# Kernel tuning notes

Measured on AMD Instinct MI355X. Metric: run time of the kernel, lower is better.

Reference implementation:

```python
import jax, jax.numpy as jnp
import numpy as np

N_NODES = 100000
N_EDGES = 1600000
N_RELS = 4
F_IN, H_DIM, OUT_DIM = 128, 64, 64
N_LAYERS = 3  # num_hidden_layers=2 h2h layers + 1 h2o layer (all 64->64 here)


def setup_inputs() -> dict:
    key = jax.random.key(0)
    ks = jax.random.split(key, 10)
    h = jax.random.normal(ks[0], (N_NODES, F_IN), dtype=jnp.float32)
    src = jax.random.randint(ks[1], (N_EDGES,), 0, N_NODES, dtype=jnp.int32)
    dst = jax.random.randint(ks[2], (N_EDGES,), 0, N_NODES, dtype=jnp.int32)
    etypes = jax.random.randint(ks[3], (N_EDGES,), 0, N_RELS, dtype=jnp.int32)
    # parameters, scaled ~1/sqrt(fan_in) for numerical sanity through ReLU stack
    W_fc = jax.random.normal(ks[4], (F_IN, H_DIM), dtype=jnp.float32) / np.sqrt(F_IN)
    W_rels = jax.random.normal(ks[5], (N_LAYERS, N_RELS, H_DIM, H_DIM), dtype=jnp.float32) / np.sqrt(H_DIM)
    W_loops = jax.random.normal(ks[6], (N_LAYERS, H_DIM, H_DIM), dtype=jnp.float32) / np.sqrt(H_DIM)
    biases = jnp.zeros((N_LAYERS, H_DIM), dtype=jnp.float32)
    W_dense = jax.random.normal(ks[7], (OUT_DIM, 1), dtype=jnp.float32) / np.sqrt(OUT_DIM)
    b_dense = jnp.zeros((1,), dtype=jnp.float32)
    return {"h": h, "src": src, "dst": dst, "etypes": etypes,
            "W_fc": W_fc, "W_rels": W_rels, "W_loops": W_loops,
            "biases": biases, "W_dense": W_dense, "b_dense": b_dense}


def reference(h, src, dst, etypes, W_fc, W_rels, W_loops, biases, W_dense, b_dense):
    n = h.shape[0]
    # GATLayer.forward returns g.ndata['z'] (fc projection); the attention
    # aggregate written to 'h' by reduce_func is never read in the original.
    x = h @ W_fc  # (N, H)
    # RelGraphConv stack: msg = W_{r(e)} h_src, sum over in-edges, + self-loop + bias, ReLU
    for l in range(N_LAYERS):
        # transform every node under every relation, then gather per edge
        xw = jnp.einsum('nd,rde->rne', x, W_rels[l])        # (R, N, H)
        msg = xw[etypes, src]                                # (E, H)
        agg = jax.ops.segment_sum(msg, dst, num_segments=n)  # (N, H)
        x = jax.nn.relu(agg + x @ W_loops[l] + biases[l])
    # SumPooling over the single graph; h viewed as (N, 1, OUT_DIM)
    pooled = jnp.sum(x.reshape(n, -1, OUT_DIM), axis=0)[None]  # (1, 1, OUT_DIM)
    out = pooled @ W_dense + b_dense                            # (1, 1, 1)
    return out
```

## Files before the change

kernel.cpp:

```cpp
#include <hip/hip_runtime.h>


typedef __attribute__((ext_vector_type(8))) short short8;
typedef __attribute__((ext_vector_type(4))) float f32x4;

__device__ inline unsigned short f32_to_bf16_rne(float x) {
  unsigned u = __builtin_bit_cast(unsigned, x);
  unsigned r = (u + 0x7FFFu + ((u >> 16) & 1u)) >> 16;
  return (unsigned short)r;
}
__device__ inline float bf16_bits_to_f32(unsigned short b) {
  unsigned u = ((unsigned)b) << 16;
  return __builtin_bit_cast(float, u);
}


__global__ void k_degree(const int* __restrict__ dst, int* __restrict__ deg, int E) {
  int i = blockIdx.x * blockDim.x + threadIdx.x;
  if (i < E) atomicAdd(&deg[dst[i]], 1);
}

__global__ __launch_bounds__(1024) void k_scan1(const int* __restrict__ deg,
                                                int* __restrict__ scan,
                                                int* __restrict__ part, int N) {
  __shared__ int s[1024];
  int tid = threadIdx.x;
  int idx = blockIdx.x * 1024 + tid;
  int v = (idx < N) ? deg[idx] : 0;
  s[tid] = v;
  __syncthreads();
  for (int off = 1; off < 1024; off <<= 1) {
    int t = (tid >= off) ? s[tid - off] : 0;
    __syncthreads();
    s[tid] += t;
    __syncthreads();
  }
  if (idx < N) scan[idx] = s[tid];
  if (tid == 1023) part[blockIdx.x] = s[1023];
}

__global__ __launch_bounds__(1024) void k_scan2(const int* __restrict__ part,
                                                int* __restrict__ partx, int nblk) {
  __shared__ int s[1024];
  int tid = threadIdx.x;
  int v = (tid < nblk) ? part[tid] : 0;
  s[tid] = v;
  __syncthreads();
  for (int off = 1; off < 1024; off <<= 1) {
    int t = (tid >= off) ? s[tid - off] : 0;
    __syncthreads();
    s[tid] += t;
    __syncthreads();
  }
  if (tid < nblk) partx[tid] = s[tid] - v;
}

__global__ void k_scan3(const int* __restrict__ scan, const int* __restrict__ deg,
                        const int* __restrict__ partx, int* __restrict__ rowptr,
                        int* __restrict__ cursor, int N, int E) {
  int i = blockIdx.x * blockDim.x + threadIdx.x;
  if (i < N) {
    int v = scan[i] - deg[i] + partx[i >> 10];
    rowptr[i] = v;
    cursor[i] = v;
  }
  if (i == 0) rowptr[N] = E;
}

__global__ void k_scatter(const int* __restrict__ src, const int* __restrict__ dst,
                          const int* __restrict__ et, int* __restrict__ cursor,
                          unsigned* __restrict__ edata, int E) {
  int i = blockIdx.x * blockDim.x + threadIdx.x;
  if (i < E) {
    int d = dst[i];
    int pos = atomicAdd(&cursor[d], 1);
    edata[pos] = (unsigned)src[i] | ((unsigned)et[i] << 17);
  }
}


__global__ __launch_bounds__(256) void k_agg(const int* __restrict__ rowptr,
                                             const unsigned* __restrict__ edata,
                                             const float* __restrict__ x,
                                             float* __restrict__ pre, int N) {
  int wid = (blockIdx.x * blockDim.x + threadIdx.x) >> 6;
  int lane = threadIdx.x & 63;
  if (wid >= N) return;
  int beg = rowptr[wid];
  int end = rowptr[wid + 1];
  float a0 = 0.f, a1 = 0.f, a2 = 0.f, a3 = 0.f;
  int e = beg;
  for (; e + 4 <= end; e += 4) {
    unsigned p0 = __builtin_amdgcn_readfirstlane(edata[e]);
    unsigned p1 = __builtin_amdgcn_readfirstlane(edata[e + 1]);
    unsigned p2 = __builtin_amdgcn_readfirstlane(edata[e + 2]);
    unsigned p3 = __builtin_amdgcn_readfirstlane(edata[e + 3]);
    float v0 = x[(size_t)(p0 & 0x1FFFF) * 64 + lane];
    float v1 = x[(size_t)(p1 & 0x1FFFF) * 64 + lane];
    float v2 = x[(size_t)(p2 & 0x1FFFF) * 64 + lane];
    float v3 = x[(size_t)(p3 & 0x1FFFF) * 64 + lane];
    { int t = p0 >> 17; if (t == 0) a0 += v0; else if (t == 1) a1 += v0; else if (t == 2) a2 += v0; else a3 += v0; }
    { int t = p1 >> 17; if (t == 0) a0 += v1; else if (t == 1) a1 += v1; else if (t == 2) a2 += v1; else a3 += v1; }
    { int t = p2 >> 17; if (t == 0) a0 += v2; else if (t == 1) a1 += v2; else if (t == 2) a2 += v2; else a3 += v2; }
    { int t = p3 >> 17; if (t == 0) a0 += v3; else if (t == 1) a1 += v3; else if (t == 2) a2 += v3; else a3 += v3; }
  }
  for (; e < end; ++e) {
    unsigned p = __builtin_amdgcn_readfirstlane(edata[e]);
    float v = x[(size_t)(p & 0x1FFFF) * 64 + lane];
    int t = p >> 17;
    if (t == 0) a0 += v; else if (t == 1) a1 += v; else if (t == 2) a2 += v; else a3 += v;
  }
  float* o = pre + (size_t)wid * 256 + lane;
  o[0] = a0; o[64] = a1; o[128] = a2; o[192] = a3;
}


__global__ void k_bconv(const float* __restrict__ B0, int K0,
                        const float* __restrict__ B1, int K1,
                        unsigned short* __restrict__ Bh,
                        unsigned short* __restrict__ Bm,
                        unsigned short* __restrict__ Bl) {
  int K = K0 + K1;
  int idx = blockIdx.x * 256 + threadIdx.x;
  if (idx >= K * 64) return;
  int k = idx >> 6, col = idx & 63;
  float v;
  if (k < K0)      v = B0[(size_t)k * 64 + col];
  else if (k < K)  v = B1[(size_t)(k - K0) * 64 + col];
  else             v = 0.f;
  int kstep = k >> 5, kk = k & 31;
  int ct = col >> 4;
  int lane = (col & 15) + (((kk >> 3)) << 4);
  int j = kk & 7;
  size_t o = (((size_t)(kstep * 4 + ct)) * 64 + lane) * 8 + j;
  unsigned short hb = f32_to_bf16_rne(v);
  float r1 = v - bf16_bits_to_f32(hb);
  unsigned short mb = f32_to_bf16_rne(r1);
  unsigned short lb = f32_to_bf16_rne(r1 - bf16_bits_to_f32(mb));
  Bh[o] = hb; Bm[o] = mb; Bl[o] = lb;
}


__global__ __launch_bounds__(256) void k_mgemm(
    const float* __restrict__ A0, int K0,
    const float* __restrict__ A1, int K1,
    const unsigned short* __restrict__ Bh,
    const unsigned short* __restrict__ Bm,
    const unsigned short* __restrict__ Bl,
    const float* __restrict__ bias, int relu,
    float* __restrict__ C, int M,
    const float* __restrict__ Wd, float* __restrict__ accum, int pool) {
  __shared__ short8 Ah[8 * 64], Am[8 * 64], Al[8 * 64];
  __shared__ float red[256];

  const int tid = threadIdx.x;
  const int wave = tid >> 6;
  const int lane = tid & 63;
  const int row0 = blockIdx.x * 128;
  const int K = K0 + K1;

  f32x4 acc[2][4];
#pragma unroll
  for (int i = 0; i < 2; ++i)
#pragma unroll
    for (int j = 0; j < 4; ++j) acc[i][j] = (f32x4){0.f, 0.f, 0.f, 0.f};

  const int srow = tid >> 1;
  const int kk0 = (tid & 1) * 16;
  const int rt_s = srow >> 4;
  const int laneA = (srow & 15) + ((kk0 >> 3) << 4);

  for (int kb = 0; kb < K; kb += 32) {
    {
      const float* Ap;
      int lda;
      if (kb < K0) { Ap = A0 + kb; lda = K0; }
      else         { Ap = A1 + (kb - K0); lda = K1; }
      const int grow = row0 + srow;
      float v[16];
      if (grow < M) {
        const float* s = Ap + (size_t)grow * lda + kk0;
#pragma unroll
        for (int q = 0; q < 4; ++q)
          *reinterpret_cast<float4*>(&v[q * 4]) =
              *reinterpret_cast<const float4*>(s + q * 4);
      } else {
#pragma unroll
        for (int q = 0; q < 16; ++q) v[q] = 0.f;
      }
      short h[16], m[16], l[16];
#pragma unroll
      for (int q = 0; q < 16; ++q) {
        unsigned short hb = f32_to_bf16_rne(v[q]);
        float r1 = v[q] - bf16_bits_to_f32(hb);
        unsigned short mb = f32_to_bf16_rne(r1);
        unsigned short lb = f32_to_bf16_rne(r1 - bf16_bits_to_f32(mb));
        h[q] = (short)hb; m[q] = (short)mb; l[q] = (short)lb;
      }
      short8 H0 = {h[0], h[1], h[2], h[3], h[4], h[5], h[6], h[7]};
      short8 H1 = {h[8], h[9], h[10], h[11], h[12], h[13], h[14], h[15]};
      short8 M0 = {m[0], m[1], m[2], m[3], m[4], m[5], m[6], m[7]};
      short8 M1 = {m[8], m[9], m[10], m[11], m[12], m[13], m[14], m[15]};
      short8 L0 = {l[0], l[1], l[2], l[3], l[4], l[5], l[6], l[7]};
      short8 L1 = {l[8], l[9], l[10], l[11], l[12], l[13], l[14], l[15]};
      Ah[rt_s * 64 + laneA] = H0;
      Ah[rt_s * 64 + laneA + 16] = H1;
      Am[rt_s * 64 + laneA] = M0;
      Am[rt_s * 64 + laneA + 16] = M1;
      Al[rt_s * 64 + laneA] = L0;
      Al[rt_s * 64 + laneA + 16] = L1;
    }
    __syncthreads();

    const int rt0 = wave * 2, rt1 = rt0 + 1;
    short8 ah0 = Ah[rt0 * 64 + lane], ah1 = Ah[rt1 * 64 + lane];
    short8 am0 = Am[rt0 * 64 + lane], am1 = Am[rt1 * 64 + lane];
    short8 al0 = Al[rt0 * 64 + lane], al1 = Al[rt1 * 64 + lane];
    const int kstep = kb >> 5;
#pragma unroll
    for (int ct = 0; ct < 4; ++ct) {
      size_t bo = (((size_t)(kstep * 4 + ct)) * 64 + lane) * 8;
      short8 bh = *reinterpret_cast<const short8*>(&Bh[bo]);
      short8 bm = *reinterpret_cast<const short8*>(&Bm[bo]);
      short8 bl = *reinterpret_cast<const short8*>(&Bl[bo]);
      acc[0][ct] = __builtin_amdgcn_mfma_f32_16x16x32_bf16(ah0, bh, acc[0][ct], 0, 0, 0);
      acc[0][ct] = __builtin_amdgcn_mfma_f32_16x16x32_bf16(ah0, bm, acc[0][ct], 0, 0, 0);
      acc[0][ct] = __builtin_amdgcn_mfma_f32_16x16x32_bf16(am0, bh, acc[0][ct], 0, 0, 0);
      acc[0][ct] = __builtin_amdgcn_mfma_f32_16x16x32_bf16(ah0, bl, acc[0][ct], 0, 0, 0);
      acc[0][ct] = __builtin_amdgcn_mfma_f32_16x16x32_bf16(al0, bh, acc[0][ct], 0, 0, 0);
      acc[0][ct] = __builtin_amdgcn_mfma_f32_16x16x32_bf16(am0, bm, acc[0][ct], 0, 0, 0);
      acc[1][ct] = __builtin_amdgcn_mfma_f32_16x16x32_bf16(ah1, bh, acc[1][ct], 0, 0, 0);
      acc[1][ct] = __builtin_amdgcn_mfma_f32_16x16x32_bf16(ah1, bm, acc[1][ct], 0, 0, 0);
      acc[1][ct] = __builtin_amdgcn_mfma_f32_16x16x32_bf16(am1, bh, acc[1][ct], 0, 0, 0);
      acc[1][ct] = __builtin_amdgcn_mfma_f32_16x16x32_bf16(ah1, bl, acc[1][ct], 0, 0, 0);
      acc[1][ct] = __builtin_amdgcn_mfma_f32_16x16x32_bf16(al1, bh, acc[1][ct], 0, 0, 0);
      acc[1][ct] = __builtin_amdgcn_mfma_f32_16x16x32_bf16(am1, bm, acc[1][ct], 0, 0, 0);
    }
    __syncthreads();
  }

  float local = 0.f;
#pragma unroll
  for (int rt = 0; rt < 2; ++rt) {
#pragma unroll
    for (int ct = 0; ct < 4; ++ct) {
      const int col = ct * 16 + (lane & 15);
      const float bc = bias ? bias[col] : 0.f;
#pragma unroll
      for (int reg = 0; reg < 4; ++reg) {
        const int grow = row0 + wave * 32 + rt * 16 + (lane >> 4) * 4 + reg;
        if (grow < M) {
          float y = acc[rt][ct][reg] + bc;
          if (relu) y = fmaxf(y, 0.f);
          if (pool) local += y * Wd[col];
          else C[(size_t)grow * 64 + col] = y;
        }
      }
    }
  }
  if (pool) {
    red[tid] = local;
    __syncthreads();
    for (int off = 128; off > 0; off >>= 1) {
      if (tid < off) red[tid] += red[tid + off];
      __syncthreads();
    }
    if (tid == 0) atomicAdd(accum, red[0]);
  }
}

__global__ void k_final(const float* __restrict__ accum, const float* __restrict__ b,
                        float* __restrict__ out) {
  out[0] = accum[0] + b[0];
}


extern "C" void kernel_launch(void* const* d_in, const int* in_sizes, int n_in,
                              void* d_out, int out_size, void* d_ws, size_t ws_size,
                              hipStream_t stream) {
  const float* h       = (const float*)d_in[0];
  const int*   src     = (const int*)d_in[1];
  const int*   dst     = (const int*)d_in[2];
  const int*   et      = (const int*)d_in[3];
  const float* W_fc    = (const float*)d_in[4];
  const float* W_rels  = (const float*)d_in[5];
  const float* W_loops = (const float*)d_in[6];
  const float* biases  = (const float*)d_in[7];
  const float* W_dense = (const float*)d_in[8];
  const float* b_dense = (const float*)d_in[9];
  float* out = (float*)d_out;

  const int N = in_sizes[0] / 128;
  const int E = in_sizes[1];

  size_t cur = 0;
  auto carve = [&](size_t bytes) -> char* {
    cur = (cur + 255) & ~(size_t)255;
    char* p = (char*)d_ws + cur;
    cur += bytes;
    return p;
  };
  int* deg        = (int*)carve((size_t)N * 4);
  int* scan       = (int*)carve((size_t)N * 4);
  int* part       = (int*)carve(1024 * 4);
  int* partx      = (int*)carve(1024 * 4);
  int* rowptr     = (int*)carve((size_t)(N + 1) * 4);
  int* cursor     = (int*)carve((size_t)N * 4);
  unsigned* edata = (unsigned*)carve((size_t)E * 4);
  float* xA       = (float*)carve((size_t)N * 64 * 4);
  float* xB       = (float*)carve((size_t)N * 64 * 4);
  float* pre      = (float*)carve((size_t)N * 256 * 4);
  float* accum    = (float*)carve(256);
  unsigned short* Bfc[3];
  for (int p = 0; p < 3; ++p) Bfc[p] = (unsigned short*)carve((size_t)128 * 64 * 2);
  unsigned short* Blay[3][3];
  for (int l = 0; l < 3; ++l)
    for (int p = 0; p < 3; ++p) Blay[l][p] = (unsigned short*)carve((size_t)320 * 64 * 2);

  hipMemsetAsync(deg, 0, (size_t)N * 4, stream);
  hipMemsetAsync(accum, 0, 4, stream);

  k_bconv<<<(128 * 64 + 255) / 256, 256, 0, stream>>>(W_fc, 128, nullptr, 0,
                                                      Bfc[0], Bfc[1], Bfc[2]);
  for (int l = 0; l < 3; ++l)
    k_bconv<<<(320 * 64 + 255) / 256, 256, 0, stream>>>(
        W_rels + (size_t)l * 4 * 64 * 64, 256, W_loops + (size_t)l * 64 * 64, 64,
        Blay[l][0], Blay[l][1], Blay[l][2]);

  const int eb = (E + 255) / 256;
  k_degree<<<eb, 256, 0, stream>>>(dst, deg, E);
  const int nblk = (N + 1023) / 1024;
  k_scan1<<<nblk, 1024, 0, stream>>>(deg, scan, part, N);
  k_scan2<<<1, 1024, 0, stream>>>(part, partx, nblk);
  k_scan3<<<(N + 255) / 256, 256, 0, stream>>>(scan, deg, partx, rowptr, cursor, N, E);
  k_scatter<<<eb, 256, 0, stream>>>(src, dst, et, cursor, edata, E);

  const int gb = (N + 127) / 128;
  k_mgemm<<<gb, 256, 0, stream>>>(h, 128, nullptr, 0,
                                  Bfc[0], Bfc[1], Bfc[2],
                                  nullptr, 0, xA, N, nullptr, nullptr, 0);

  float* xin = xA;
  float* xout = xB;
  for (int l = 0; l < 3; ++l) {
    k_agg<<<(N + 3) / 4, 256, 0, stream>>>(rowptr, edata, xin, pre, N);
    const int last = (l == 2);
    k_mgemm<<<gb, 256, 0, stream>>>(pre, 256, xin, 64,
                                    Blay[l][0], Blay[l][1], Blay[l][2],
                                    biases + (size_t)l * 64, 1,
                                    last ? nullptr : xout, N,
                                    last ? W_dense : nullptr, accum, last);
    float* t = xin; xin = xout; xout = t;
  }

  k_final<<<1, 1, 0, stream>>>(accum, b_dense, out);
}
```

Baseline: 667.6 us.

## Fuse edge aggregation with relation GEMM into one per-layer kernel

```diff
diff --git a/kernel.cpp b/kernel.cpp
--- a/kernel.cpp
+++ b/kernel.cpp
@@ -76,42 +76,6 @@
     int pos = atomicAdd(&cursor[d], 1);
     edata[pos] = (unsigned)src[i] | ((unsigned)et[i] << 17);
   }
-}
-
-
-__global__ __launch_bounds__(256) void k_agg(const int* __restrict__ rowptr,
-                                             const unsigned* __restrict__ edata,
-                                             const float* __restrict__ x,
-                                             float* __restrict__ pre, int N) {
-  int wid = (blockIdx.x * blockDim.x + threadIdx.x) >> 6;
-  int lane = threadIdx.x & 63;
-  if (wid >= N) return;
-  int beg = rowptr[wid];
-  int end = rowptr[wid + 1];
-  float a0 = 0.f, a1 = 0.f, a2 = 0.f, a3 = 0.f;
-  int e = beg;
-  for (; e + 4 <= end; e += 4) {
-    unsigned p0 = __builtin_amdgcn_readfirstlane(edata[e]);
-    unsigned p1 = __builtin_amdgcn_readfirstlane(edata[e + 1]);
-    unsigned p2 = __builtin_amdgcn_readfirstlane(edata[e + 2]);
-    unsigned p3 = __builtin_amdgcn_readfirstlane(edata[e + 3]);
-    float v0 = x[(size_t)(p0 & 0x1FFFF) * 64 + lane];
-    float v1 = x[(size_t)(p1 & 0x1FFFF) * 64 + lane];
-    float v2 = x[(size_t)(p2 & 0x1FFFF) * 64 + lane];
-    float v3 = x[(size_t)(p3 & 0x1FFFF) * 64 + lane];
-    { int t = p0 >> 17; if (t == 0) a0 += v0; else if (t == 1) a1 += v0; else if (t == 2) a2 += v0; else a3 += v0; }
-    { int t = p1 >> 17; if (t == 0) a0 += v1; else if (t == 1) a1 += v1; else if (t == 2) a2 += v1; else a3 += v1; }
-    { int t = p2 >> 17; if (t == 0) a0 += v2; else if (t == 1) a1 += v2; else if (t == 2) a2 += v2; else a3 += v2; }
-    { int t = p3 >> 17; if (t == 0) a0 += v3; else if (t == 1) a1 += v3; else if (t == 2) a2 += v3; else a3 += v3; }
-  }
-  for (; e < end; ++e) {
-    unsigned p = __builtin_amdgcn_readfirstlane(edata[e]);
-    float v = x[(size_t)(p & 0x1FFFF) * 64 + lane];
-    int t = p >> 17;
-    if (t == 0) a0 += v; else if (t == 1) a1 += v; else if (t == 2) a2 += v; else a3 += v;
-  }
-  float* o = pre + (size_t)wid * 256 + lane;
-  o[0] = a0; o[64] = a1; o[128] = a2; o[192] = a3;
 }
 
 
@@ -141,23 +105,132 @@
 }
 
 
-__global__ __launch_bounds__(256) void k_mgemm(
-    const float* __restrict__ A0, int K0,
-    const float* __restrict__ A1, int K1,
+__global__ __launch_bounds__(256) void k_fused(
+    const int* __restrict__ rowptr, const unsigned* __restrict__ edata,
+    const float* __restrict__ x,
     const unsigned short* __restrict__ Bh,
     const unsigned short* __restrict__ Bm,
     const unsigned short* __restrict__ Bl,
-    const float* __restrict__ bias, int relu,
-    float* __restrict__ C, int M,
+    const float* __restrict__ bias,
+    float* __restrict__ xout, int N,
     const float* __restrict__ Wd, float* __restrict__ accum, int pool) {
+  __shared__ float A[16][324];
+  __shared__ float red[256];
+
+  const int tid = threadIdx.x;
+  const int wave = tid >> 6;
+  const int lane = tid & 63;
+  const int node0 = blockIdx.x * 16;
+
+  for (int i = 0; i < 4; ++i) {
+    const int r = wave * 4 + i;
+    const int n = node0 + r;
+    float a0 = 0.f, a1 = 0.f, a2 = 0.f, a3 = 0.f, xs = 0.f;
+    if (n < N) {
+      int beg = rowptr[n];
+      int end = rowptr[n + 1];
+      int e = beg;
+      for (; e + 4 <= end; e += 4) {
+        unsigned p0 = __builtin_amdgcn_readfirstlane(edata[e]);
+        unsigned p1 = __builtin_amdgcn_readfirstlane(edata[e + 1]);
+        unsigned p2 = __builtin_amdgcn_readfirstlane(edata[e + 2]);
+        unsigned p3 = __builtin_amdgcn_readfirstlane(edata[e + 3]);
+        float v0 = x[(size_t)(p0 & 0x1FFFF) * 64 + lane];
+        float v1 = x[(size_t)(p1 & 0x1FFFF) * 64 + lane];
+        float v2 = x[(size_t)(p2 & 0x1FFFF) * 64 + lane];
+        float v3 = x[(size_t)(p3 & 0x1FFFF) * 64 + lane];
+        { int t = p0 >> 17; if (t == 0) a0 += v0; else if (t == 1) a1 += v0; else if (t == 2) a2 += v0; else a3 += v0; }
+        { int t = p1 >> 17; if (t == 0) a0 += v1; else if (t == 1) a1 += v1; else if (t == 2) a2 += v1; else a3 += v1; }
+        { int t = p2 >> 17; if (t == 0) a0 += v2; else if (t == 1) a1 += v2; else if (t == 2) a2 += v2; else a3 += v2; }
+        { int t = p3 >> 17; if (t == 0) a0 += v3; else if (t == 1) a1 += v3; else if (t == 2) a2 += v3; else a3 += v3; }
+      }
+      for (; e < end; ++e) {
+        unsigned p = __builtin_amdgcn_readfirstlane(edata[e]);
+        float v = x[(size_t)(p & 0x1FFFF) * 64 + lane];
+        int t = p >> 17;
+        if (t == 0) a0 += v; else if (t == 1) a1 += v; else if (t == 2) a2 += v; else a3 += v;
+      }
+      xs = x[(size_t)n * 64 + lane];
+    }
+    A[r][0 * 64 + lane] = a0;
+    A[r][1 * 64 + lane] = a1;
+    A[r][2 * 64 + lane] = a2;
+    A[r][3 * 64 + lane] = a3;
+    A[r][256 + lane] = xs;
+  }
+  __syncthreads();
+
+  f32x4 acc = (f32x4){0.f, 0.f, 0.f, 0.f};
+  const int arow = lane & 15;
+  const int koff = (lane >> 4) * 8;
+#pragma unroll
+  for (int ks = 0; ks < 10; ++ks) {
+    float av[8];
+    *reinterpret_cast<float4*>(&av[0]) =
+        *reinterpret_cast<const float4*>(&A[arow][ks * 32 + koff]);
+    *reinterpret_cast<float4*>(&av[4]) =
+        *reinterpret_cast<const float4*>(&A[arow][ks * 32 + koff + 4]);
+    short h[8], m[8], l[8];
+#pragma unroll
+    for (int q = 0; q < 8; ++q) {
+      unsigned short hb = f32_to_bf16_rne(av[q]);
+      float r1 = av[q] - bf16_bits_to_f32(hb);
+      unsigned short mb = f32_to_bf16_rne(r1);
+      unsigned short lb = f32_to_bf16_rne(r1 - bf16_bits_to_f32(mb));
+      h[q] = (short)hb; m[q] = (short)mb; l[q] = (short)lb;
+    }
+    short8 ah = {h[0], h[1], h[2], h[3], h[4], h[5], h[6], h[7]};
+    short8 am = {m[0], m[1], m[2], m[3], m[4], m[5], m[6], m[7]};
+    short8 al = {l[0], l[1], l[2], l[3], l[4], l[5], l[6], l[7]};
+    size_t bo = (((size_t)(ks * 4 + wave)) * 64 + lane) * 8;
+    short8 bh = *reinterpret_cast<const short8*>(&Bh[bo]);
+    short8 bm = *reinterpret_cast<const short8*>(&Bm[bo]);
+    short8 bl = *reinterpret_cast<const short8*>(&Bl[bo]);
+    acc = __builtin_amdgcn_mfma_f32_16x16x32_bf16(ah, bh, acc, 0, 0, 0);
+    acc = __builtin_amdgcn_mfma_f32_16x16x32_bf16(ah, bm, acc, 0, 0, 0);
+    acc = __builtin_amdgcn_mfma_f32_16x16x32_bf16(am, bh, acc, 0, 0, 0);
+    acc = __builtin_amdgcn_mfma_f32_16x16x32_bf16(ah, bl, acc, 0, 0, 0);
+    acc = __builtin_amdgcn_mfma_f32_16x16x32_bf16(al, bh, acc, 0, 0, 0);
+    acc = __builtin_amdgcn_mfma_f32_16x16x32_bf16(am, bm, acc, 0, 0, 0);
+  }
+
+  const int col = wave * 16 + (lane & 15);
+  const float bc = bias ? bias[col] : 0.f;
+  float local = 0.f;
+#pragma unroll
+  for (int reg = 0; reg < 4; ++reg) {
+    const int grow = node0 + (lane >> 4) * 4 + reg;
+    if (grow < N) {
+      float y = fmaxf(acc[reg] + bc, 0.f);
+      if (pool) local += y * Wd[col];
+      else xout[(size_t)grow * 64 + col] = y;
+    }
+  }
+  if (pool) {
+    red[tid] = local;
+    __syncthreads();
+    for (int off = 128; off > 0; off >>= 1) {
+      if (tid < off) red[tid] += red[tid + off];
+      __syncthreads();
+    }
+    if (tid == 0) atomicAdd(accum, red[0]);
+  }
+}
+
+
+__global__ __launch_bounds__(256) void k_mgemm(
+    const float* __restrict__ A0, int K0,
+    const unsigned short* __restrict__ Bh,
+    const unsigned short* __restrict__ Bm,
+    const unsigned short* __restrict__ Bl,
+    float* __restrict__ C, int M) {
   __shared__ short8 Ah[8 * 64], Am[8 * 64], Al[8 * 64];
-  __shared__ float red[256];
 
   const int tid = threadIdx.x;
   const int wave = tid >> 6;
   const int lane = tid & 63;
   const int row0 = blockIdx.x * 128;
-  const int K = K0 + K1;
+  const int K = K0;
 
   f32x4 acc[2][4];
 #pragma unroll
@@ -172,14 +245,10 @@
 
   for (int kb = 0; kb < K; kb += 32) {
     {
-      const float* Ap;
-      int lda;
-      if (kb < K0) { Ap = A0 + kb; lda = K0; }
-      else         { Ap = A1 + (kb - K0); lda = K1; }
       const int grow = row0 + srow;
       float v[16];
       if (grow < M) {
-        const float* s = Ap + (size_t)grow * lda + kk0;
+        const float* s = A0 + (size_t)grow * K + kb + kk0;
 #pragma unroll
         for (int q = 0; q < 4; ++q)
           *reinterpret_cast<float4*>(&v[q * 4]) =
@@ -239,33 +308,17 @@
     __syncthreads();
   }
 
-  float local = 0.f;
 #pragma unroll
   for (int rt = 0; rt < 2; ++rt) {
 #pragma unroll
     for (int ct = 0; ct < 4; ++ct) {
       const int col = ct * 16 + (lane & 15);
-      const float bc = bias ? bias[col] : 0.f;
 #pragma unroll
       for (int reg = 0; reg < 4; ++reg) {
         const int grow = row0 + wave * 32 + rt * 16 + (lane >> 4) * 4 + reg;
-        if (grow < M) {
-          float y = acc[rt][ct][reg] + bc;
-          if (relu) y = fmaxf(y, 0.f);
-          if (pool) local += y * Wd[col];
-          else C[(size_t)grow * 64 + col] = y;
-        }
+        if (grow < M) C[(size_t)grow * 64 + col] = acc[rt][ct][reg];
       }
     }
-  }
-  if (pool) {
-    red[tid] = local;
-    __syncthreads();
-    for (int off = 128; off > 0; off >>= 1) {
-      if (tid < off) red[tid] += red[tid + off];
-      __syncthreads();
-    }
-    if (tid == 0) atomicAdd(accum, red[0]);
   }
 }
 
@@ -309,7 +362,6 @@
   unsigned* edata = (unsigned*)carve((size_t)E * 4);
   float* xA       = (float*)carve((size_t)N * 64 * 4);
   float* xB       = (float*)carve((size_t)N * 64 * 4);
-  float* pre      = (float*)carve((size_t)N * 256 * 4);
   float* accum    = (float*)carve(256);
   unsigned short* Bfc[3];
   for (int p = 0; p < 3; ++p) Bfc[p] = (unsigned short*)carve((size_t)128 * 64 * 2);
@@ -336,18 +388,16 @@
   k_scatter<<<eb, 256, 0, stream>>>(src, dst, et, cursor, edata, E);
 
   const int gb = (N + 127) / 128;
-  k_mgemm<<<gb, 256, 0, stream>>>(h, 128, nullptr, 0,
-                                  Bfc[0], Bfc[1], Bfc[2],
-                                  nullptr, 0, xA, N, nullptr, nullptr, 0);
-
+  k_mgemm<<<gb, 256, 0, stream>>>(h, 128, Bfc[0], Bfc[1], Bfc[2], xA, N);
+
+  const int fb = (N + 15) / 16;
   float* xin = xA;
   float* xout = xB;
   for (int l = 0; l < 3; ++l) {
-    k_agg<<<(N + 3) / 4, 256, 0, stream>>>(rowptr, edata, xin, pre, N);
     const int last = (l == 2);
-    k_mgemm<<<gb, 256, 0, stream>>>(pre, 256, xin, 64,
+    k_fused<<<fb, 256, 0, stream>>>(rowptr, edata, xin,
                                     Blay[l][0], Blay[l][1], Blay[l][2],
-                                    biases + (size_t)l * 64, 1,
+                                    biases + (size_t)l * 64,
                                     last ? nullptr : xout, N,
                                     last ? W_dense : nullptr, accum, last);
     float* t = xin; xin = xout; xout = t;
```

Result: slower. 710.6 us (+6.4%).
